# Kernel tuning notes

Hardware: AMD Instinct MI355X
Metric: run time of the kernel (lower is better)

The kernel has to match this reference:

```python
import jax, jax.numpy as jnp
import numpy as np

B, T, CH, Hs, Ws = 2, 64, 512, 24, 24
DIM = CH // 2          # 256, attention channel dim
HEADS = 8
HEAD_DIM = DIM // HEADS  # 32
MAX_SEQ = 64


def setup_inputs() -> dict:
    key = jax.random.key(0)
    ks = jax.random.split(key, 6)
    return {
        "x": jax.random.normal(ks[0], (B, T, CH, Hs, Ws), dtype=jnp.float32),
        "rpb_table": jax.random.normal(ks[1], (2 * MAX_SEQ - 1, HEADS), dtype=jnp.float32) * 0.02,
        "qkv_w": jax.random.normal(ks[2], (3 * DIM, DIM), dtype=jnp.float32) * 0.02,
        "qkv_b": jax.random.normal(ks[3], (3 * DIM,), dtype=jnp.float32) * 0.02,
        "proj_w": jax.random.normal(ks[4], (DIM, DIM), dtype=jnp.float32) * 0.02,
        "proj_b": jax.random.normal(ks[5], (DIM,), dtype=jnp.float32) * 0.02,
    }


def reference(x, rpb_table, qkv_w, qkv_b, proj_w, proj_b):
    b, t, c, h, w = x.shape
    half = c // 2
    a_part = x[:, :, :half]       # (B,T,half,H,W) untouched branch
    b_part = x[:, :, half:]       # attention branch

    # 'b t c h w -> (b h w) t c'
    xb = jnp.transpose(b_part, (0, 3, 4, 1, 2)).reshape(b * h * w, t, half)
    B_, N, C = xb.shape
    scale = HEAD_DIM ** -0.5

    qkv = xb @ qkv_w.T + qkv_b                        # (B_, N, 3*C)
    qkv = qkv.reshape(B_, N, 3, HEADS, HEAD_DIM)
    qkv = jnp.transpose(qkv, (2, 0, 3, 1, 4))          # (3, B_, heads, N, hd)
    q, k, v = qkv[0] * scale, qkv[1], qkv[2]

    attn = jnp.einsum('bhnd,bhmd->bhnm', q, k)         # (B_, heads, N, N)

    # relative position bias: index = p2 - p1 + (MAX_SEQ - 1)
    pos = jnp.arange(t)
    rel_idx = pos[None, :] - pos[:, None] + (MAX_SEQ - 1)   # (N, N)
    bias = rpb_table[rel_idx]                              # (N, N, heads)
    bias = jnp.transpose(bias, (2, 0, 1))                  # (heads, N, N)
    attn = attn + bias[None]

    # causal (mask_future=True): -inf strictly above the diagonal
    causal = jnp.where(pos[None, :] > pos[:, None], -jnp.inf, 0.0).astype(attn.dtype)
    attn = attn + causal[None, None]

    attn = jax.nn.softmax(attn, axis=-1)

    out = jnp.einsum('bhnm,bhmd->bhnd', attn, v)       # (B_, heads, N, hd)
    out = jnp.transpose(out, (0, 2, 1, 3)).reshape(B_, N, C)
    out = out @ proj_w.T + proj_b

    # '(b h w) t c -> b t c h w'
    out = out.reshape(b, h, w, t, half)
    out = jnp.transpose(out, (0, 3, 4, 1, 2))

    return jnp.concatenate([a_part, out], axis=2)
```

## Files before the change

### kernel.cpp

```cpp
#include <hip/hip_runtime.h>
#include <hip/hip_bf16.h>

typedef __attribute__((ext_vector_type(4))) float  f32x4;
typedef __attribute__((ext_vector_type(8))) short  bf16x8;
typedef __attribute__((ext_vector_type(8))) unsigned short u16x8;
typedef __attribute__((ext_vector_type(4))) unsigned short u16x4;
typedef __attribute__((ext_vector_type(4))) int i32x4;

__device__ __forceinline__ unsigned short f2bf(float f) {
    union { float f; unsigned u; } v; v.f = f;
    unsigned u = v.u;
    unsigned r = u + 0x7fffu + ((u >> 16) & 1u);
    return (unsigned short)(r >> 16);
}

__device__ __forceinline__ unsigned cvtpk(float lo, float hi) {
    unsigned r;
    asm("v_cvt_pk_bf16_f32 %0, %1, %2" : "=v"(r) : "v"(lo), "v"(hi));
    return r;
}

__device__ __forceinline__ int selshfl(unsigned lo, unsigned hiw, int srcLane, bool hi) {
    int a = __shfl((int)lo, srcLane, 64);
    int b = __shfl((int)hiw, srcLane, 64);
    return hi ? b : a;
}

__device__ __forceinline__ bf16x8 mkfrag(int w0, int w1, int w2, int w3) {
    i32x4 t; t[0] = w0; t[1] = w1; t[2] = w2; t[3] = w3;
    return __builtin_bit_cast(bf16x8, t);
}

__device__ __forceinline__ void gload16(const void* g, void* l) {
    __builtin_amdgcn_global_load_lds((const __attribute__((address_space(1))) unsigned*)g,
                                     (__attribute__((address_space(3))) unsigned*)l, 16, 0, 0);
}

#define MFMA(A, B, C) __builtin_amdgcn_mfma_f32_16x16x32_bf16((A), (B), (C), 0, 0, 0)


__global__ void cvt_weights(const float* __restrict__ qkv_w, const float* __restrict__ proj_w,
                            unsigned short* __restrict__ wq, unsigned short* __restrict__ wp) {
    int i = blockIdx.x * 256 + threadIdx.x;
    if (i < 196608) wq[i] = f2bf(qkv_w[i]);
    else            wp[i - 196608] = f2bf(proj_w[i - 196608]);
}

__global__ __launch_bounds__(256) void transpose_b(const float* __restrict__ x,
                                                   unsigned short* __restrict__ xb,
                                                   float* __restrict__ outp) {
    __shared__ unsigned short tile[256][72];
    const int bt  = blockIdx.x;
    const int hw0 = blockIdx.y * 64;
    const int tid = threadIdx.x;
    {
        const size_t slab = (size_t)bt * 294912;
        #pragma unroll
        for (int it = 0; it < 16; ++it) {
            int idx = it * 256 + tid;
            int ch  = idx >> 4;
            int off = (idx & 15) * 4;
            size_t o = slab + (size_t)ch * 576 + hw0 + off;
            *(float4*)(outp + o) = *(const float4*)(x + o);
        }
    }
    const float* src = x + ((size_t)bt * 512 + 256) * 576 + hw0;
    const int c_sub = tid >> 4, l16 = tid & 15;
    #pragma unroll
    for (int it = 0; it < 16; ++it) {
        int cc = it * 16 + c_sub;
        const float4 v = *(const float4*)(src + (size_t)cc * 576 + l16 * 4);
        tile[cc][l16 * 4 + 0] = f2bf(v.x);
        tile[cc][l16 * 4 + 1] = f2bf(v.y);
        tile[cc][l16 * 4 + 2] = f2bf(v.z);
        tile[cc][l16 * 4 + 3] = f2bf(v.w);
    }
    __syncthreads();
    const int row = tid >> 2;
    const int cs  = (tid & 3) * 64;
    const int b = bt >> 6, t = bt & 63;
    size_t m = ((size_t)(b * 576 + hw0 + row)) * 64 + t;
    unsigned short* dst = xb + m * 256 + cs;
    #pragma unroll
    for (int q = 0; q < 8; ++q) {
        u16x8 v;
        #pragma unroll
        for (int u = 0; u < 8; ++u) v[u] = tile[cs + q * 8 + u][row];
        *(u16x8*)(dst + q * 8) = v;
    }
}

#define PKPAIR(D, A, B4) \
    const unsigned D##_0 = cvtpk(A[0] + B4.x, A[1] + B4.y); \
    const unsigned D##_1 = cvtpk(A[2] + B4.z, A[3] + B4.w);

#define MKF(DST, LO, HI_) \
    DST = mkfrag(selshfl(LO##_0, HI_##_0, lA, hi), selshfl(LO##_1, HI_##_1, lA, hi), \
                 selshfl(LO##_0, HI_##_0, lB, hi), selshfl(LO##_1, HI_##_1, lB, hi));

#define SM1(SC, JT, R) { \
    const int j_ = (JT) * 16 + 4 * g + (R); \
    int d_ = j_ - i_ + 63; d_ = d_ > 63 ? 63 : d_; \
    const float v_ = SC[R] * scale + bias_w[d_]; \
    const float e_ = (j_ > i_) ? 0.f : __expf(v_); \
    SC[R] = e_; rs += e_; }

#define SMROW(SC, JT) SM1(SC, JT, 0) SM1(SC, JT, 1) SM1(SC, JT, 2) SM1(SC, JT, 3)

#define ATT_COL(IT, QF, O0V, O1V) { \
    f32x4 Sc0{0.f,0.f,0.f,0.f}, Sc1{0.f,0.f,0.f,0.f}, Sc2{0.f,0.f,0.f,0.f}, Sc3{0.f,0.f,0.f,0.f}; \
    Sc0 = MFMA(kf0, QF, Sc0); Sc1 = MFMA(kf1, QF, Sc1); \
    Sc2 = MFMA(kf2, QF, Sc2); Sc3 = MFMA(kf3, QF, Sc3); \
    const int i_ = (IT) * 16 + c; \
    float rs = 0.f; \
    SMROW(Sc0, 0) SMROW(Sc1, 1) SMROW(Sc2, 2) SMROW(Sc3, 3) \
    rs += __shfl_xor(rs, 16, 64); \
    rs += __shfl_xor(rs, 32, 64); \
    const float inv = 1.0f / rs; \
    const unsigned p00 = cvtpk(Sc0[0]*inv, Sc0[1]*inv), p01 = cvtpk(Sc0[2]*inv, Sc0[3]*inv); \
    const unsigned p10 = cvtpk(Sc1[0]*inv, Sc1[1]*inv), p11 = cvtpk(Sc1[2]*inv, Sc1[3]*inv); \
    const unsigned p20 = cvtpk(Sc2[0]*inv, Sc2[1]*inv), p21 = cvtpk(Sc2[2]*inv, Sc2[3]*inv); \
    const unsigned p30 = cvtpk(Sc3[0]*inv, Sc3[1]*inv), p31 = cvtpk(Sc3[2]*inv, Sc3[3]*inv); \
    const bf16x8 pf0 = mkfrag(selshfl(p00, p10, lA, hi), selshfl(p01, p11, lA, hi), \
                              selshfl(p00, p10, lB, hi), selshfl(p01, p11, lB, hi)); \
    const bf16x8 pf1 = mkfrag(selshfl(p20, p30, lA, hi), selshfl(p21, p31, lA, hi), \
                              selshfl(p20, p30, lB, hi), selshfl(p21, p31, lB, hi)); \
    O0V = MFMA(vf00, pf0, O0V); O1V = MFMA(vf10, pf0, O1V); \
    O0V = MFMA(vf01, pf1, O0V); O1V = MFMA(vf11, pf1, O1V); }

#define OSTOREG(OV, DT, IT) { \
    const int t_ = (IT) * 16 + c; \
    u16x4 v_; v_[0] = f2bf(OV[0]); v_[1] = f2bf(OV[1]); v_[2] = f2bf(OV[2]); v_[3] = f2bf(OV[3]); \
    *(u16x4*)(att + ((size_t)(t_ * 1152 + p)) * 256 + h * 32 + (DT) * 16 + 4 * g) = v_; }

__global__ __launch_bounds__(256, 3)
void attn_heads(
    const unsigned short* __restrict__ xb,
    const unsigned short* __restrict__ wqkv,
    const float* __restrict__ qkv_b,
    const float* __restrict__ rpb,
    unsigned short* __restrict__ att)
{
    __shared__ unsigned short vt[4][32 * 88];
    __shared__ float bias_s[8][64];

    const int tid  = threadIdx.x;
    const int lane = tid & 63, w = tid >> 6;
    const int c = lane & 15, g = lane >> 4;
    const bool hi = g >= 2;
    const int lA = c + 16 * ((2 * g) & 3);
    const int lB = c + 16 * ((2 * g + 1) & 3);

    bias_s[tid & 7][tid >> 3] = rpb[tid];
    bias_s[(tid + 256) & 7][(tid + 256) >> 3] = rpb[tid + 256];
    __syncthreads();

    const int gw = blockIdx.x * 4 + w;
    const int h  = gw / 1152;
    const int p  = gw - h * 1152;
    const float* bias_w = bias_s[h];
    const float scale = 0.17677669529663687f;
    const unsigned short* xrow = xb + (size_t)p * 16384;
    unsigned short* vts = vt[w];

    f32x4 aq[2][4] = {}, ak[2][4] = {}, av[2][4] = {};
    #pragma unroll
    for (int ks = 0; ks < 8; ++ks) {
        bf16x8 bx[4];
        #pragma unroll
        for (int b2 = 0; b2 < 4; ++b2)
            bx[b2] = *(const bf16x8*)(xrow + (b2 * 16 + c) * 256 + ks * 32 + g * 8);
        #pragma unroll
        for (int a2 = 0; a2 < 2; ++a2) {
            const size_t ko = (size_t)ks * 32 + g * 8;
            const bf16x8 fq = *(const bf16x8*)(wqkv + (size_t)(      h * 32 + a2 * 16 + c) * 256 + ko);
            const bf16x8 fk = *(const bf16x8*)(wqkv + (size_t)(256 + h * 32 + a2 * 16 + c) * 256 + ko);
            const bf16x8 fv = *(const bf16x8*)(wqkv + (size_t)(512 + h * 32 + a2 * 16 + c) * 256 + ko);
            #pragma unroll
            for (int b2 = 0; b2 < 4; ++b2) {
                aq[a2][b2] = MFMA(fq, bx[b2], aq[a2][b2]);
                ak[a2][b2] = MFMA(fk, bx[b2], ak[a2][b2]);
                av[a2][b2] = MFMA(fv, bx[b2], av[a2][b2]);
            }
        }
    }

    #pragma unroll
    for (int a2 = 0; a2 < 2; ++a2) {
        float4 bv = *(const float4*)(qkv_b + 512 + h * 32 + a2 * 16 + g * 4);
        #pragma unroll
        for (int b2 = 0; b2 < 4; ++b2) {
            int t = b2 * 16 + c;
            vts[(a2 * 16 + g * 4 + 0) * 88 + t] = f2bf(av[a2][b2][0] + bv.x);
            vts[(a2 * 16 + g * 4 + 1) * 88 + t] = f2bf(av[a2][b2][1] + bv.y);
            vts[(a2 * 16 + g * 4 + 2) * 88 + t] = f2bf(av[a2][b2][2] + bv.z);
            vts[(a2 * 16 + g * 4 + 3) * 88 + t] = f2bf(av[a2][b2][3] + bv.w);
        }
    }

    bf16x8 kf0, kf1, kf2, kf3, qf0, qf1, qf2, qf3;
    {
        const float4 bk0 = *(const float4*)(qkv_b + 256 + h * 32 + g * 4);
        const float4 bk1 = *(const float4*)(qkv_b + 256 + h * 32 + 16 + g * 4);
        const float4 bq0 = *(const float4*)(qkv_b +       h * 32 + g * 4);
        const float4 bq1 = *(const float4*)(qkv_b +       h * 32 + 16 + g * 4);
        PKPAIR(kp00, ak[0][0], bk0) PKPAIR(kp01, ak[0][1], bk0)
        PKPAIR(kp02, ak[0][2], bk0) PKPAIR(kp03, ak[0][3], bk0)
        PKPAIR(kp10, ak[1][0], bk1) PKPAIR(kp11, ak[1][1], bk1)
        PKPAIR(kp12, ak[1][2], bk1) PKPAIR(kp13, ak[1][3], bk1)
        PKPAIR(qp00, aq[0][0], bq0) PKPAIR(qp01, aq[0][1], bq0)
        PKPAIR(qp02, aq[0][2], bq0) PKPAIR(qp03, aq[0][3], bq0)
        PKPAIR(qp10, aq[1][0], bq1) PKPAIR(qp11, aq[1][1], bq1)
        PKPAIR(qp12, aq[1][2], bq1) PKPAIR(qp13, aq[1][3], bq1)
        MKF(kf0, kp00, kp10) MKF(kf1, kp01, kp11) MKF(kf2, kp02, kp12) MKF(kf3, kp03, kp13)
        MKF(qf0, qp00, qp10) MKF(qf1, qp01, qp11) MKF(qf2, qp02, qp12) MKF(qf3, qp03, qp13)
    }

    const bf16x8 vf00 = *(const bf16x8*)(&vts[( 0 + c) * 88 +  0 + g * 8]);
    const bf16x8 vf01 = *(const bf16x8*)(&vts[( 0 + c) * 88 + 32 + g * 8]);
    const bf16x8 vf10 = *(const bf16x8*)(&vts[(16 + c) * 88 +  0 + g * 8]);
    const bf16x8 vf11 = *(const bf16x8*)(&vts[(16 + c) * 88 + 32 + g * 8]);

    f32x4 O00{0.f,0.f,0.f,0.f}, O01{0.f,0.f,0.f,0.f}, O02{0.f,0.f,0.f,0.f}, O03{0.f,0.f,0.f,0.f};
    f32x4 O10{0.f,0.f,0.f,0.f}, O11{0.f,0.f,0.f,0.f}, O12{0.f,0.f,0.f,0.f}, O13{0.f,0.f,0.f,0.f};
    ATT_COL(0, qf0, O00, O10)
    ATT_COL(1, qf1, O01, O11)
    ATT_COL(2, qf2, O02, O12)
    ATT_COL(3, qf3, O03, O13)

    OSTOREG(O00, 0, 0) OSTOREG(O01, 0, 1) OSTOREG(O02, 0, 2) OSTOREG(O03, 0, 3)
    OSTOREG(O10, 1, 0) OSTOREG(O11, 1, 1) OSTOREG(O12, 1, 2) OSTOREG(O13, 1, 3)
}

__global__ __launch_bounds__(256, 4) void gemm_proj(const unsigned short* __restrict__ A,
                                                    const unsigned short* __restrict__ Wt,
                                                    const float* __restrict__ bias,
                                                    float* __restrict__ out) {
    __shared__ unsigned short Ws[128 * 64];
    __shared__ unsigned short Xs[128 * 64];
    const int m0 = blockIdx.x * 128, n0 = blockIdx.y * 128;
    const int tid = threadIdx.x;
    const int lane = tid & 63, w = tid >> 6;
    const int wy = w >> 1, wx = w & 1;
    const int c = lane & 15, g = lane >> 4;
    const int lr = lane >> 3, lu = lane & 7;
    const int su = lu ^ lr;
    const int cs7 = c & 7;
    f32x4 acc[4][4] = {};
    for (int k0 = 0; k0 < 256; k0 += 64) {
        #pragma unroll
        for (int q = 0; q < 4; ++q) {
            int R = w * 32 + q * 8;
            gload16(Wt + (size_t)(n0 + R + lr) * 256 + k0 + su * 8, &Ws[R * 64]);
            gload16(A  + (size_t)(m0 + R + lr) * 256 + k0 + su * 8, &Xs[R * 64]);
        }
        __syncthreads();
        #pragma unroll
        for (int kk = 0; kk < 2; ++kk) {
            bf16x8 af[4], bx[4];
            #pragma unroll
            for (int a2 = 0; a2 < 4; ++a2)
                af[a2] = *(const bf16x8*)(&Ws[(wy * 64 + a2 * 16 + c) * 64 + (((kk * 4 + g) ^ cs7) * 8)]);
            #pragma unroll
            for (int b2 = 0; b2 < 4; ++b2)
                bx[b2] = *(const bf16x8*)(&Xs[(wx * 64 + b2 * 16 + c) * 64 + (((kk * 4 + g) ^ cs7) * 8)]);
            #pragma unroll
            for (int a2 = 0; a2 < 4; ++a2)
                #pragma unroll
                for (int b2 = 0; b2 < 4; ++b2)
                    acc[a2][b2] = MFMA(af[a2], bx[b2], acc[a2][b2]);
        }
        __syncthreads();
    }
    #pragma unroll
    for (int a2 = 0; a2 < 4; ++a2) {
        int n = n0 + wy * 64 + a2 * 16 + g * 4;
        float4 bv = *(const float4*)(bias + n);
        #pragma unroll
        for (int b2 = 0; b2 < 4; ++b2) {
            int m = m0 + wx * 64 + b2 * 16 + c;
            int t   = m / 1152;
            int rem = m % 1152;
            int bb  = rem / 576;
            int hw  = rem % 576;
            float* dst = out + ((size_t)(bb * 64 + t) * 512 + 256 + n) * 576 + hw;
            dst[0]        = acc[a2][b2][0] + bv.x;
            dst[576]      = acc[a2][b2][1] + bv.y;
            dst[2 * 576]  = acc[a2][b2][2] + bv.z;
            dst[3 * 576]  = acc[a2][b2][3] + bv.w;
        }
    }
}

extern "C" void kernel_launch(void* const* d_in, const int* in_sizes, int n_in,
                              void* d_out, int out_size, void* d_ws, size_t ws_size,
                              hipStream_t stream) {
    (void)in_sizes; (void)n_in; (void)out_size;
    const float* x      = (const float*)d_in[0];
    const float* rpb    = (const float*)d_in[1];
    const float* qkv_w  = (const float*)d_in[2];
    const float* qkv_b  = (const float*)d_in[3];
    const float* proj_w = (const float*)d_in[4];
    const float* proj_b = (const float*)d_in[5];
    float* out = (float*)d_out;

    char* ws = (char*)d_ws;
    unsigned short* wq  = (unsigned short*)ws;
    unsigned short* wp  = (unsigned short*)(ws + 393216);
    unsigned short* xb  = (unsigned short*)(ws + 524288);
    unsigned short* att = (unsigned short*)(ws + 524288 + 37748736);
    if (ws_size < (size_t)524288 + 2 * 37748736) return;

    cvt_weights<<<1024, 256, 0, stream>>>(qkv_w, proj_w, wq, wp);
    transpose_b<<<dim3(128, 9), 256, 0, stream>>>(x, xb, out);
    attn_heads<<<2304, 256, 0, stream>>>(xb, wq, qkv_b, rpb, att);
    gemm_proj<<<dim3(576, 2), 256, 0, stream>>>(att, wp, proj_b, out);
}
```

Measured before the change: 227.5 us.

## Map 8 heads of one pixel per block and split QKV projection phases

Each block now has 512 threads and handles one spatial position, with one wave per head, so all 8 heads of a position share the same x row in cache. Block index is swizzled across positions. The fused Q/K/V projection loop is split into a V pass (written to LDS) followed by a K/Q pass, which cuts live accumulator registers and allows the higher occupancy target of 4. The cost is that the x row is read twice per wave and LDS use per block doubles.

After: 251.6 us. +10.6%, slower.

```diff
diff --git a/kernel.cpp b/kernel.cpp
--- a/kernel.cpp
+++ b/kernel.cpp
@@ -133,7 +133,7 @@
     u16x4 v_; v_[0] = f2bf(OV[0]); v_[1] = f2bf(OV[1]); v_[2] = f2bf(OV[2]); v_[3] = f2bf(OV[3]); \
     *(u16x4*)(att + ((size_t)(t_ * 1152 + p)) * 256 + h * 32 + (DT) * 16 + 4 * g) = v_; }
 
-__global__ __launch_bounds__(256, 3)
+__global__ __launch_bounds__(512, 4)
 void attn_heads(
     const unsigned short* __restrict__ xb,
     const unsigned short* __restrict__ wqkv,
@@ -141,7 +141,7 @@
     const float* __restrict__ rpb,
     unsigned short* __restrict__ att)
 {
-    __shared__ unsigned short vt[4][32 * 88];
+    __shared__ unsigned short vt[8][32 * 88];
     __shared__ float bias_s[8][64];
 
     const int tid  = threadIdx.x;
@@ -152,54 +152,66 @@
     const int lB = c + 16 * ((2 * g + 1) & 3);
 
     bias_s[tid & 7][tid >> 3] = rpb[tid];
-    bias_s[(tid + 256) & 7][(tid + 256) >> 3] = rpb[tid + 256];
     __syncthreads();
 
-    const int gw = blockIdx.x * 4 + w;
-    const int h  = gw / 1152;
-    const int p  = gw - h * 1152;
+    const int h  = w;
+    const int bid = blockIdx.x;
+    const int p  = (bid & 7) * 144 + (bid >> 3);
     const float* bias_w = bias_s[h];
     const float scale = 0.17677669529663687f;
     const unsigned short* xrow = xb + (size_t)p * 16384;
     unsigned short* vts = vt[w];
 
-    f32x4 aq[2][4] = {}, ak[2][4] = {}, av[2][4] = {};
-    #pragma unroll
-    for (int ks = 0; ks < 8; ++ks) {
-        bf16x8 bx[4];
-        #pragma unroll
-        for (int b2 = 0; b2 < 4; ++b2)
-            bx[b2] = *(const bf16x8*)(xrow + (b2 * 16 + c) * 256 + ks * 32 + g * 8);
+    {
+        f32x4 av[2][4] = {};
+        #pragma unroll
+        for (int ks = 0; ks < 8; ++ks) {
+            bf16x8 bx[4];
+            #pragma unroll
+            for (int b2 = 0; b2 < 4; ++b2)
+                bx[b2] = *(const bf16x8*)(xrow + (b2 * 16 + c) * 256 + ks * 32 + g * 8);
+            #pragma unroll
+            for (int a2 = 0; a2 < 2; ++a2) {
+                const bf16x8 fv = *(const bf16x8*)(wqkv + (size_t)(512 + h * 32 + a2 * 16 + c) * 256 + ks * 32 + g * 8);
+                #pragma unroll
+                for (int b2 = 0; b2 < 4; ++b2)
+                    av[a2][b2] = MFMA(fv, bx[b2], av[a2][b2]);
+            }
+        }
         #pragma unroll
         for (int a2 = 0; a2 < 2; ++a2) {
-            const size_t ko = (size_t)ks * 32 + g * 8;
-            const bf16x8 fq = *(const bf16x8*)(wqkv + (size_t)(      h * 32 + a2 * 16 + c) * 256 + ko);
-            const bf16x8 fk = *(const bf16x8*)(wqkv + (size_t)(256 + h * 32 + a2 * 16 + c) * 256 + ko);
-            const bf16x8 fv = *(const bf16x8*)(wqkv + (size_t)(512 + h * 32 + a2 * 16 + c) * 256 + ko);
+            float4 bv = *(const float4*)(qkv_b + 512 + h * 32 + a2 * 16 + g * 4);
             #pragma unroll
             for (int b2 = 0; b2 < 4; ++b2) {
-                aq[a2][b2] = MFMA(fq, bx[b2], aq[a2][b2]);
-                ak[a2][b2] = MFMA(fk, bx[b2], ak[a2][b2]);
-                av[a2][b2] = MFMA(fv, bx[b2], av[a2][b2]);
+                int t = b2 * 16 + c;
+                vts[(a2 * 16 + g * 4 + 0) * 88 + t] = f2bf(av[a2][b2][0] + bv.x);
+                vts[(a2 * 16 + g * 4 + 1) * 88 + t] = f2bf(av[a2][b2][1] + bv.y);
+                vts[(a2 * 16 + g * 4 + 2) * 88 + t] = f2bf(av[a2][b2][2] + bv.z);
+                vts[(a2 * 16 + g * 4 + 3) * 88 + t] = f2bf(av[a2][b2][3] + bv.w);
             }
-        }
-    }
-
-    #pragma unroll
-    for (int a2 = 0; a2 < 2; ++a2) {
-        float4 bv = *(const float4*)(qkv_b + 512 + h * 32 + a2 * 16 + g * 4);
-        #pragma unroll
-        for (int b2 = 0; b2 < 4; ++b2) {
-            int t = b2 * 16 + c;
-            vts[(a2 * 16 + g * 4 + 0) * 88 + t] = f2bf(av[a2][b2][0] + bv.x);
-            vts[(a2 * 16 + g * 4 + 1) * 88 + t] = f2bf(av[a2][b2][1] + bv.y);
-            vts[(a2 * 16 + g * 4 + 2) * 88 + t] = f2bf(av[a2][b2][2] + bv.z);
-            vts[(a2 * 16 + g * 4 + 3) * 88 + t] = f2bf(av[a2][b2][3] + bv.w);
         }
     }
 
     bf16x8 kf0, kf1, kf2, kf3, qf0, qf1, qf2, qf3;
     {
+        f32x4 ak[2][4] = {}, aq[2][4] = {};
+        #pragma unroll
+        for (int ks = 0; ks < 8; ++ks) {
+            bf16x8 bx[4];
+            #pragma unroll
+            for (int b2 = 0; b2 < 4; ++b2)
+                bx[b2] = *(const bf16x8*)(xrow + (b2 * 16 + c) * 256 + ks * 32 + g * 8);
+            #pragma unroll
+            for (int a2 = 0; a2 < 2; ++a2) {
+                const bf16x8 fk = *(const bf16x8*)(wqkv + (size_t)(256 + h * 32 + a2 * 16 + c) * 256 + ks * 32 + g * 8);
+                const bf16x8 fq = *(const bf16x8*)(wqkv + (size_t)(      h * 32 + a2 * 16 + c) * 256 + ks * 32 + g * 8);
+                #pragma unroll
+                for (int b2 = 0; b2 < 4; ++b2) {
+                    ak[a2][b2] = MFMA(fk, bx[b2], ak[a2][b2]);
+                    aq[a2][b2] = MFMA(fq, bx[b2], aq[a2][b2]);
+                }
+            }
+        }
         const float4 bk0 = *(const float4*)(qkv_b + 256 + h * 32 + g * 4);
         const float4 bk1 = *(const float4*)(qkv_b + 256 + h * 32 + 16 + g * 4);
         const float4 bq0 = *(const float4*)(qkv_b +       h * 32 + g * 4);
@@ -313,6 +325,6 @@
 
     cvt_weights<<<1024, 256, 0, stream>>>(qkv_w, proj_w, wq, wp);
     transpose_b<<<dim3(128, 9), 256, 0, stream>>>(x, xb, out);
-    attn_heads<<<2304, 256, 0, stream>>>(xb, wq, qkv_b, rpb, att);
+    attn_heads<<<1152, 512, 0, stream>>>(xb, wq, qkv_b, rpb, att);
     gemm_proj<<<dim3(576, 2), 256, 0, stream>>>(att, wp, proj_b, out);
 }
```
